# Kernel tuning notes

Hardware: AMD Instinct MI355X
Metric: run time of the kernel (lower is better)

Reference implementation:

```python
import jax, jax.numpy as jnp
import numpy as np

N = 8192       # num_nodes
E = 262144     # num_edges (avg degree 32)
D_IN = 256
D_H = 256
D_OUT = 256
BN_EPS = 1e-5


def _linear_params(key, din, dout):
    # torch nn.Linear default init: U(-1/sqrt(din), 1/sqrt(din))
    s = 1.0 / np.sqrt(din)
    kw, kb = jax.random.split(key)
    W = jax.random.uniform(kw, (dout, din), jnp.float32, -s, s)
    b = jax.random.uniform(kb, (dout,), jnp.float32, -s, s)
    return W, b


def setup_inputs() -> dict:
    key = jax.random.key(0)
    ks = jax.random.split(key, 6)
    x = jax.random.normal(ks[0], (N, D_IN), jnp.float32)
    edge_index = jax.random.randint(ks[1], (2, E), 0, N, dtype=jnp.int64)
    W1, b1 = _linear_params(ks[2], D_IN, D_H)
    W2, b2 = _linear_params(ks[3], D_H, D_H)
    W3, b3 = _linear_params(ks[4], D_H, D_OUT)
    return {
        "x": x, "edge_index": edge_index,
        "W1": W1, "b1": b1, "W2": W2, "b2": b2, "W3": W3, "b3": b3,
        "g1": jnp.ones((D_H,), jnp.float32), "be1": jnp.zeros((D_H,), jnp.float32),
        "g2": jnp.ones((D_H,), jnp.float32), "be2": jnp.zeros((D_H,), jnp.float32),
        "g3": jnp.ones((D_OUT,), jnp.float32), "be3": jnp.zeros((D_OUT,), jnp.float32),
    }


def _build_norm(edge_index):
    # add self loops, scatter 1.0 into dense NxN adjacency (duplicates collapse via set)
    loop = jnp.arange(N, dtype=edge_index.dtype)
    rows = jnp.concatenate([edge_index[0], loop])
    cols = jnp.concatenate([edge_index[1], loop])
    adj = jnp.zeros((N, N), jnp.float32).at[rows, cols].set(1.0)
    deg = adj.sum(axis=1)
    dinv = jnp.where(deg > 0, deg ** -0.5, 0.0)  # inf -> 0 as in original
    return dinv[:, None] * adj * dinv[None, :]


def _gcn(x, norm, W, b):
    # linear then symmetric-normalized aggregation
    return norm @ (x @ W.T + b)


def _bn(x, g, b):
    # BatchNorm1d with batch statistics (biased var), eps=1e-5
    mu = x.mean(axis=0)
    var = x.var(axis=0)
    return (x - mu) * jax.lax.rsqrt(var + BN_EPS) * g + b


def reference(x, edge_index, W1, b1, W2, b2, W3, b3, g1, be1, g2, be2, g3, be3):
    norm = _build_norm(edge_index)
    h = jax.nn.relu(_bn(_gcn(x, norm, W1, b1), g1, be1))
    h = jax.nn.relu(_bn(_gcn(h, norm, W2, b2), g2, be2))
    h = _bn(_gcn(h, norm, W3, b3), g3, be3)
    return h
```

## Files before the change

### kernel.cpp

```cpp
#include <hip/hip_runtime.h>

#define N_NODES 8192
#define N_EDGES 262144
#define D 256
#define ADJ_WORDS 256
#define MAX_DEG 128
#define AGG_BLOCKS 2048
#define RED_BLOCKS 128

typedef __attribute__((ext_vector_type(8))) short bf16x8;
typedef __attribute__((ext_vector_type(4))) float f32x4;

__device__ __forceinline__ short f2bf(float f) {
    unsigned u = __builtin_bit_cast(unsigned, f);
    u += 0x7fffu + ((u >> 16) & 1);
    return (short)(u >> 16);
}
__device__ __forceinline__ float bf2f(unsigned short u) {
    return __builtin_bit_cast(float, ((unsigned)u) << 16);
}

__global__ void build_adj(const int* __restrict__ ei, unsigned* __restrict__ adj,
                          int* __restrict__ deg) {
    int i = blockIdx.x * blockDim.x + threadIdx.x;
    int r, c;
    if (i < N_EDGES) {
        r = ei[i];
        c = ei[N_EDGES + i];
    } else if (i < N_EDGES + N_NODES) {
        r = i - N_EDGES;
        c = r;
    } else {
        return;
    }
    unsigned bit = 1u << (c & 31);
    unsigned old = atomicOr(&adj[r * ADJ_WORDS + (c >> 5)], bit);
    if (!(old & bit)) atomicAdd(&deg[r], 1);
}

__global__ __launch_bounds__(256) void compute_dinv(const int* __restrict__ deg,
                                                    float* __restrict__ dinv) {
    int i = blockIdx.x * 256 + threadIdx.x;
    int d = deg[i];
    dinv[i] = d > 0 ? rsqrtf((float)d) : 0.0f;
}

__global__ __launch_bounds__(256) void build_nbrs(const unsigned* __restrict__ adj,
                                                  const float* __restrict__ dinv,
                                                  int* __restrict__ nbr_idx,
                                                  float* __restrict__ nbr_w,
                                                  const float* __restrict__ W1,
                                                  const float* __restrict__ W2,
                                                  const float* __restrict__ W3,
                                                  unsigned short* __restrict__ Wb1,
                                                  unsigned short* __restrict__ Wb2,
                                                  unsigned short* __restrict__ Wb3) {
    if (blockIdx.x >= N_NODES) {
        int i = (blockIdx.x - N_NODES) * 256 + threadIdx.x;
        int which = i >> 16, j = i & 65535;
        const float* src = which == 0 ? W1 : which == 1 ? W2 : W3;
        unsigned short* dst = which == 0 ? Wb1 : which == 1 ? Wb2 : Wb3;
        dst[j] = (unsigned short)f2bf(src[j]);
        return;
    }
    const int r = blockIdx.x;
    const int t = threadIdx.x;
    const int lane = t & 63, wave = t >> 6;
    unsigned m = adj[r * ADJ_WORDS + t];
    int cnt = __popc(m);
    int x = cnt;
    #pragma unroll
    for (int off = 1; off < 64; off <<= 1) {
        int v = __shfl_up(x, off, 64);
        if (lane >= off) x += v;
    }
    __shared__ int wtot[4];
    if (lane == 63) wtot[wave] = x;
    __syncthreads();
    int woff = 0;
    #pragma unroll
    for (int w = 0; w < 4; w++) woff += (w < wave) ? wtot[w] : 0;
    int base = woff + x - cnt;
    const float dr = dinv[r];
    int* oi = nbr_idx + (size_t)r * MAX_DEG;
    float* ow = nbr_w + (size_t)r * MAX_DEG;
    while (m) {
        int b = __ffs(m) - 1;
        m &= m - 1;
        int c = (t << 5) + b;
        if (base < MAX_DEG) {
            oi[base] = c;
            ow[base] = dr * dinv[c];
        }
        base++;
    }
}

template <bool APPLY, bool RELU>
__global__ __launch_bounds__(256) void gemm_mfma(const float* __restrict__ Xsrc,
                                                 const float* __restrict__ scale,
                                                 const float* __restrict__ shift,
                                                 const unsigned short* __restrict__ Wb,
                                                 const float* __restrict__ bias,
                                                 unsigned short* __restrict__ Hb) {
    const int bn = blockIdx.x * 64;
    const int bm = blockIdx.y * 128;
    const int tid = threadIdx.x;
    const int wave = tid >> 6, lane = tid & 63;
    const int l16 = lane & 15, q = lane >> 4;
    const int mrow0 = bm + wave * 32;

    f32x4 acc[2][4];
    #pragma unroll
    for (int i = 0; i < 2; i++)
        #pragma unroll
        for (int j = 0; j < 4; j++) acc[i][j] = (f32x4){0.f, 0.f, 0.f, 0.f};

    for (int k0 = 0; k0 < D; k0 += 32) {
        const int kq = k0 + q * 8;
        bf16x8 xb[2];
        float4 sc0, sc1, sh0, sh1;
        if (APPLY) {
            sc0 = *(const float4*)(scale + kq);
            sc1 = *(const float4*)(scale + kq + 4);
            sh0 = *(const float4*)(shift + kq);
            sh1 = *(const float4*)(shift + kq + 4);
        }
        #pragma unroll
        for (int mf = 0; mf < 2; mf++) {
            const float* xr = Xsrc + (size_t)(mrow0 + mf * 16 + l16) * D + kq;
            float4 a = *(const float4*)xr;
            float4 b = *(const float4*)(xr + 4);
            float v[8] = {a.x, a.y, a.z, a.w, b.x, b.y, b.z, b.w};
            if (APPLY) {
                float sc[8] = {sc0.x, sc0.y, sc0.z, sc0.w, sc1.x, sc1.y, sc1.z, sc1.w};
                float sh[8] = {sh0.x, sh0.y, sh0.z, sh0.w, sh1.x, sh1.y, sh1.z, sh1.w};
                #pragma unroll
                for (int j = 0; j < 8; j++) {
                    v[j] = fmaf(v[j], sc[j], sh[j]);
                    if (RELU) v[j] = fmaxf(v[j], 0.0f);
                }
            }
            #pragma unroll
            for (int j = 0; j < 8; j++) xb[mf][j] = f2bf(v[j]);
        }
        #pragma unroll
        for (int nf = 0; nf < 4; nf++) {
            bf16x8 wa = *(const bf16x8*)(Wb + (size_t)(bn + nf * 16 + l16) * D + kq);
            #pragma unroll
            for (int mf = 0; mf < 2; mf++)
                acc[mf][nf] = __builtin_amdgcn_mfma_f32_16x16x32_bf16(wa, xb[mf], acc[mf][nf], 0, 0, 0);
        }
    }

    #pragma unroll
    for (int mf = 0; mf < 2; mf++) {
        const int m = mrow0 + mf * 16 + l16;
        #pragma unroll
        for (int nf = 0; nf < 4; nf++) {
            const int nb = bn + nf * 16 + q * 4;
            float4 b4 = *(const float4*)(bias + nb);
            short4 o;
            o.x = f2bf(acc[mf][nf][0] + b4.x);
            o.y = f2bf(acc[mf][nf][1] + b4.y);
            o.z = f2bf(acc[mf][nf][2] + b4.z);
            o.w = f2bf(acc[mf][nf][3] + b4.w);
            *(short4*)(Hb + (size_t)m * D + nb) = o;
        }
    }
}

__global__ __launch_bounds__(256) void aggregate_bf16(const int* __restrict__ nbr_idx,
                                                      const float* __restrict__ nbr_w,
                                                      const int* __restrict__ deg,
                                                      const unsigned short* __restrict__ Hb,
                                                      float* __restrict__ G,
                                                      float* __restrict__ psum,
                                                      float* __restrict__ psumsq) {
    const int wave = threadIdx.x >> 6;
    const int lane = threadIdx.x & 63;
    const int ch = lane * 4;
    const int r = blockIdx.x * 4 + wave;

    int dg = deg[r]; if (dg > MAX_DEG) dg = MAX_DEG;
    const int* idx = nbr_idx + (size_t)r * MAX_DEG;
    const float* wt = nbr_w + (size_t)r * MAX_DEG;
    float4 A = make_float4(0.f, 0.f, 0.f, 0.f);
    int j = 0;
    for (; j + 8 <= dg; j += 8) {
        int4 c0 = *(const int4*)(idx + j);
        int4 c1 = *(const int4*)(idx + j + 4);
        float4 w0 = *(const float4*)(wt + j);
        float4 w1 = *(const float4*)(wt + j + 4);
        ushort4 u0 = *(const ushort4*)(Hb + (size_t)c0.x * D + ch);
        ushort4 u1 = *(const ushort4*)(Hb + (size_t)c0.y * D + ch);
        ushort4 u2 = *(const ushort4*)(Hb + (size_t)c0.z * D + ch);
        ushort4 u3 = *(const ushort4*)(Hb + (size_t)c0.w * D + ch);
        ushort4 u4 = *(const ushort4*)(Hb + (size_t)c1.x * D + ch);
        ushort4 u5 = *(const ushort4*)(Hb + (size_t)c1.y * D + ch);
        ushort4 u6 = *(const ushort4*)(Hb + (size_t)c1.z * D + ch);
        ushort4 u7 = *(const ushort4*)(Hb + (size_t)c1.w * D + ch);
        A.x = fmaf(w0.x, bf2f(u0.x), A.x); A.y = fmaf(w0.x, bf2f(u0.y), A.y);
        A.z = fmaf(w0.x, bf2f(u0.z), A.z); A.w = fmaf(w0.x, bf2f(u0.w), A.w);
        A.x = fmaf(w0.y, bf2f(u1.x), A.x); A.y = fmaf(w0.y, bf2f(u1.y), A.y);
        A.z = fmaf(w0.y, bf2f(u1.z), A.z); A.w = fmaf(w0.y, bf2f(u1.w), A.w);
        A.x = fmaf(w0.z, bf2f(u2.x), A.x); A.y = fmaf(w0.z, bf2f(u2.y), A.y);
        A.z = fmaf(w0.z, bf2f(u2.z), A.z); A.w = fmaf(w0.z, bf2f(u2.w), A.w);
        A.x = fmaf(w0.w, bf2f(u3.x), A.x); A.y = fmaf(w0.w, bf2f(u3.y), A.y);
        A.z = fmaf(w0.w, bf2f(u3.z), A.z); A.w = fmaf(w0.w, bf2f(u3.w), A.w);
        A.x = fmaf(w1.x, bf2f(u4.x), A.x); A.y = fmaf(w1.x, bf2f(u4.y), A.y);
        A.z = fmaf(w1.x, bf2f(u4.z), A.z); A.w = fmaf(w1.x, bf2f(u4.w), A.w);
        A.x = fmaf(w1.y, bf2f(u5.x), A.x); A.y = fmaf(w1.y, bf2f(u5.y), A.y);
        A.z = fmaf(w1.y, bf2f(u5.z), A.z); A.w = fmaf(w1.y, bf2f(u5.w), A.w);
        A.x = fmaf(w1.z, bf2f(u6.x), A.x); A.y = fmaf(w1.z, bf2f(u6.y), A.y);
        A.z = fmaf(w1.z, bf2f(u6.z), A.z); A.w = fmaf(w1.z, bf2f(u6.w), A.w);
        A.x = fmaf(w1.w, bf2f(u7.x), A.x); A.y = fmaf(w1.w, bf2f(u7.y), A.y);
        A.z = fmaf(w1.w, bf2f(u7.z), A.z); A.w = fmaf(w1.w, bf2f(u7.w), A.w);
    }
    for (; j + 4 <= dg; j += 4) {
        int4 c0 = *(const int4*)(idx + j);
        float4 w0 = *(const float4*)(wt + j);
        ushort4 u0 = *(const ushort4*)(Hb + (size_t)c0.x * D + ch);
        ushort4 u1 = *(const ushort4*)(Hb + (size_t)c0.y * D + ch);
        ushort4 u2 = *(const ushort4*)(Hb + (size_t)c0.z * D + ch);
        ushort4 u3 = *(const ushort4*)(Hb + (size_t)c0.w * D + ch);
        A.x = fmaf(w0.x, bf2f(u0.x), A.x); A.y = fmaf(w0.x, bf2f(u0.y), A.y);
        A.z = fmaf(w0.x, bf2f(u0.z), A.z); A.w = fmaf(w0.x, bf2f(u0.w), A.w);
        A.x = fmaf(w0.y, bf2f(u1.x), A.x); A.y = fmaf(w0.y, bf2f(u1.y), A.y);
        A.z = fmaf(w0.y, bf2f(u1.z), A.z); A.w = fmaf(w0.y, bf2f(u1.w), A.w);
        A.x = fmaf(w0.z, bf2f(u2.x), A.x); A.y = fmaf(w0.z, bf2f(u2.y), A.y);
        A.z = fmaf(w0.z, bf2f(u2.z), A.z); A.w = fmaf(w0.z, bf2f(u2.w), A.w);
        A.x = fmaf(w0.w, bf2f(u3.x), A.x); A.y = fmaf(w0.w, bf2f(u3.y), A.y);
        A.z = fmaf(w0.w, bf2f(u3.z), A.z); A.w = fmaf(w0.w, bf2f(u3.w), A.w);
    }
    for (; j < dg; j++) {
        int c = idx[j];
        float w = wt[j];
        ushort4 u = *(const ushort4*)(Hb + (size_t)c * D + ch);
        A.x = fmaf(w, bf2f(u.x), A.x); A.y = fmaf(w, bf2f(u.y), A.y);
        A.z = fmaf(w, bf2f(u.z), A.z); A.w = fmaf(w, bf2f(u.w), A.w);
    }
    *(float4*)(G + (size_t)r * D + ch) = A;

    __shared__ float ls[4][256], lss[4][256];
    ls[wave][ch] = A.x; ls[wave][ch + 1] = A.y; ls[wave][ch + 2] = A.z; ls[wave][ch + 3] = A.w;
    lss[wave][ch] = A.x * A.x; lss[wave][ch + 1] = A.y * A.y;
    lss[wave][ch + 2] = A.z * A.z; lss[wave][ch + 3] = A.w * A.w;
    __syncthreads();
    const int t = threadIdx.x;
    psum[blockIdx.x * 256 + t] = ls[0][t] + ls[1][t] + ls[2][t] + ls[3][t];
    psumsq[blockIdx.x * 256 + t] = lss[0][t] + lss[1][t] + lss[2][t] + lss[3][t];
}

__global__ __launch_bounds__(256) void reduce_partials(const float* __restrict__ psum,
                                                       const float* __restrict__ psumsq,
                                                       float* __restrict__ psum2,
                                                       float* __restrict__ psumsq2) {
    const int b = blockIdx.x;
    const int t = threadIdx.x;
    const int rows = AGG_BLOCKS / RED_BLOCKS;
    float s = 0.0f, q = 0.0f;
    #pragma unroll
    for (int i = 0; i < rows; i++) {
        s += psum[(size_t)(b * rows + i) * 256 + t];
        q += psumsq[(size_t)(b * rows + i) * 256 + t];
    }
    psum2[b * 256 + t] = s;
    psumsq2[b * 256 + t] = q;
}

__global__ __launch_bounds__(1024) void bn_stats2(const float* __restrict__ psum2,
                                                  const float* __restrict__ psumsq2,
                                                  const float* __restrict__ g,
                                                  const float* __restrict__ be,
                                                  float* __restrict__ scale,
                                                  float* __restrict__ shift) {
    const int t = threadIdx.x;
    const int chn = t & 255, part = t >> 8;
    float s = 0.0f, q = 0.0f;
    for (int i = part; i < RED_BLOCKS; i += 4) {
        s += psum2[i * 256 + chn];
        q += psumsq2[i * 256 + chn];
    }
    __shared__ float as[4][256], aq[4][256];
    as[part][chn] = s;
    aq[part][chn] = q;
    __syncthreads();
    if (t < 256) {
        s = as[0][t] + as[1][t] + as[2][t] + as[3][t];
        q = aq[0][t] + aq[1][t] + aq[2][t] + aq[3][t];
        float mu = s * (1.0f / N_NODES);
        float var = q * (1.0f / N_NODES) - mu * mu;
        float rstd = rsqrtf(var + 1e-5f);
        float sc = g[t] * rstd;
        scale[t] = sc;
        shift[t] = be[t] - mu * sc;
    }
}

__global__ __launch_bounds__(256) void bn_apply_out(const float* __restrict__ G,
                                                    const float* __restrict__ scale,
                                                    const float* __restrict__ shift,
                                                    float* __restrict__ Out) {
    int i = (blockIdx.x * 256 + threadIdx.x) * 4;
    int d = i & (D - 1);
    float4 v = *(const float4*)(G + i);
    float4 sc = *(const float4*)(scale + d);
    float4 sh = *(const float4*)(shift + d);
    v.x = fmaf(v.x, sc.x, sh.x);
    v.y = fmaf(v.y, sc.y, sh.y);
    v.z = fmaf(v.z, sc.z, sh.z);
    v.w = fmaf(v.w, sc.w, sh.w);
    *(float4*)(Out + i) = v;
}

extern "C" void kernel_launch(void* const* d_in, const int* in_sizes, int n_in,
                              void* d_out, int out_size, void* d_ws, size_t ws_size,
                              hipStream_t stream) {
    const float* x  = (const float*)d_in[0];
    const int*   ei = (const int*)d_in[1];
    const float* W1 = (const float*)d_in[2];
    const float* b1 = (const float*)d_in[3];
    const float* W2 = (const float*)d_in[4];
    const float* b2 = (const float*)d_in[5];
    const float* W3 = (const float*)d_in[6];
    const float* b3 = (const float*)d_in[7];
    const float* g1 = (const float*)d_in[8];
    const float* be1 = (const float*)d_in[9];
    const float* g2 = (const float*)d_in[10];
    const float* be2 = (const float*)d_in[11];
    const float* g3 = (const float*)d_in[12];
    const float* be3 = (const float*)d_in[13];

    char* ws = (char*)d_ws;
    unsigned*       adj  = (unsigned*)ws;
    unsigned short* Hb   = (unsigned short*)ws;
    int*            deg  = (int*)(ws + (8 << 20));
    float*          dinv = (float*)(ws + (8 << 20) + (32 << 10));
    float*          scale= (float*)(ws + (8 << 20) + (64 << 10));
    float*          shift= (float*)(ws + (8 << 20) + (68 << 10));
    float*          psum2= (float*)(ws + (8 << 20) + (72 << 10));
    float*          psq2 = (float*)(ws + (8 << 20) + (200 << 10));
    unsigned short* Wb1  = (unsigned short*)(ws + (8 << 20) + (330 << 10));
    unsigned short* Wb2  = (unsigned short*)(ws + (8 << 20) + (458 << 10));
    unsigned short* Wb3  = (unsigned short*)(ws + (8 << 20) + (586 << 10));
    float*          psum = (float*)(ws + (9 << 20));
    float*          psq  = (float*)(ws + (11 << 20));
    int*            nbr_idx = (int*)  (ws + (13 << 20));
    float*          nbr_w   = (float*)(ws + (17 << 20));
    float*          G       = (float*)(ws + (21 << 20));

    hipMemsetAsync(ws, 0, (8 << 20) + (32 << 10), stream);

    build_adj<<<(N_EDGES + N_NODES + 255) / 256, 256, 0, stream>>>(ei, adj, deg);
    compute_dinv<<<N_NODES / 256, 256, 0, stream>>>(deg, dinv);
    build_nbrs<<<N_NODES + 768, 256, 0, stream>>>(adj, dinv, nbr_idx, nbr_w,
                                                  W1, W2, W3, Wb1, Wb2, Wb3);

    dim3 ggrid(D / 64, N_NODES / 128);

    gemm_mfma<false, false><<<ggrid, 256, 0, stream>>>(x, nullptr, nullptr, Wb1, b1, Hb);
    aggregate_bf16<<<AGG_BLOCKS, 256, 0, stream>>>(nbr_idx, nbr_w, deg, Hb, G, psum, psq);
    reduce_partials<<<RED_BLOCKS, 256, 0, stream>>>(psum, psq, psum2, psq2);
    bn_stats2<<<1, 1024, 0, stream>>>(psum2, psq2, g1, be1, scale, shift);

    gemm_mfma<true, true><<<ggrid, 256, 0, stream>>>(G, scale, shift, Wb2, b2, Hb);
    aggregate_bf16<<<AGG_BLOCKS, 256, 0, stream>>>(nbr_idx, nbr_w, deg, Hb, G, psum, psq);
    reduce_partials<<<RED_BLOCKS, 256, 0, stream>>>(psum, psq, psum2, psq2);
    bn_stats2<<<1, 1024, 0, stream>>>(psum2, psq2, g2, be2, scale, shift);

    gemm_mfma<true, true><<<ggrid, 256, 0, stream>>>(G, scale, shift, Wb3, b3, Hb);
    aggregate_bf16<<<AGG_BLOCKS, 256, 0, stream>>>(nbr_idx, nbr_w, deg, Hb, G, psum, psq);
    reduce_partials<<<RED_BLOCKS, 256, 0, stream>>>(psum, psq, psum2, psq2);
    bn_stats2<<<1, 1024, 0, stream>>>(psum2, psq2, g3, be3, scale, shift);

    bn_apply_out<<<N_NODES * D / 1024, 256, 0, stream>>>(G, scale, shift, (float*)d_out);
}
```

Measured before the change: 255.7 us.

## Fold BN stats and dinv computation into consumer kernels, removing small launches

Removes the compute_dinv kernel by computing rsqrt of degree inline in build_nbrs, and removes the three single-block bn_stats2 kernels. Each consumer block (gemm_mfma with APPLY, and bn_apply_out) now reduces the 128 partial sums itself and builds scale/shift in shared memory. bn_apply_out is restructured so each block handles 64 rows. The aim is to cut four kernel launches and the serialized single-block reduction, at the cost of every GEMM block redundantly reading the 256 KB of partials. The deg>0 guard is dropped, which is safe here because self-loops make every degree at least 1.

```diff
diff --git a/kernel.cpp b/kernel.cpp
--- a/kernel.cpp
+++ b/kernel.cpp
@@ -38,15 +38,8 @@
     if (!(old & bit)) atomicAdd(&deg[r], 1);
 }
 
-__global__ __launch_bounds__(256) void compute_dinv(const int* __restrict__ deg,
-                                                    float* __restrict__ dinv) {
-    int i = blockIdx.x * 256 + threadIdx.x;
-    int d = deg[i];
-    dinv[i] = d > 0 ? rsqrtf((float)d) : 0.0f;
-}
-
 __global__ __launch_bounds__(256) void build_nbrs(const unsigned* __restrict__ adj,
-                                                  const float* __restrict__ dinv,
+                                                  const int* __restrict__ deg,
                                                   int* __restrict__ nbr_idx,
                                                   float* __restrict__ nbr_w,
                                                   const float* __restrict__ W1,
@@ -81,7 +74,7 @@
     #pragma unroll
     for (int w = 0; w < 4; w++) woff += (w < wave) ? wtot[w] : 0;
     int base = woff + x - cnt;
-    const float dr = dinv[r];
+    const float dr = rsqrtf((float)deg[r]);
     int* oi = nbr_idx + (size_t)r * MAX_DEG;
     float* ow = nbr_w + (size_t)r * MAX_DEG;
     while (m) {
@@ -90,7 +83,7 @@
         int c = (t << 5) + b;
         if (base < MAX_DEG) {
             oi[base] = c;
-            ow[base] = dr * dinv[c];
+            ow[base] = dr * rsqrtf((float)deg[c]);
         }
         base++;
     }
@@ -98,14 +91,33 @@
 
 template <bool APPLY, bool RELU>
 __global__ __launch_bounds__(256) void gemm_mfma(const float* __restrict__ Xsrc,
-                                                 const float* __restrict__ scale,
-                                                 const float* __restrict__ shift,
+                                                 const float* __restrict__ psum2,
+                                                 const float* __restrict__ psq2,
+                                                 const float* __restrict__ g,
+                                                 const float* __restrict__ be,
                                                  const unsigned short* __restrict__ Wb,
                                                  const float* __restrict__ bias,
                                                  unsigned short* __restrict__ Hb) {
+    __shared__ float ssc[256], ssh[256];
+    const int tid = threadIdx.x;
+    if (APPLY) {
+        float s = 0.f, q = 0.f;
+        #pragma unroll 8
+        for (int i = 0; i < RED_BLOCKS; i++) {
+            s += psum2[i * 256 + tid];
+            q += psq2[i * 256 + tid];
+        }
+        float mu = s * (1.0f / N_NODES);
+        float var = q * (1.0f / N_NODES) - mu * mu;
+        float rstd = rsqrtf(var + 1e-5f);
+        float sc = g[tid] * rstd;
+        ssc[tid] = sc;
+        ssh[tid] = be[tid] - mu * sc;
+        __syncthreads();
+    }
+
     const int bn = blockIdx.x * 64;
     const int bm = blockIdx.y * 128;
-    const int tid = threadIdx.x;
     const int wave = tid >> 6, lane = tid & 63;
     const int l16 = lane & 15, q = lane >> 4;
     const int mrow0 = bm + wave * 32;
@@ -121,10 +133,10 @@
         bf16x8 xb[2];
         float4 sc0, sc1, sh0, sh1;
         if (APPLY) {
-            sc0 = *(const float4*)(scale + kq);
-            sc1 = *(const float4*)(scale + kq + 4);
-            sh0 = *(const float4*)(shift + kq);
-            sh1 = *(const float4*)(shift + kq + 4);
+            sc0 = *(const float4*)(ssc + kq);
+            sc1 = *(const float4*)(ssc + kq + 4);
+            sh0 = *(const float4*)(ssh + kq);
+            sh1 = *(const float4*)(ssh + kq + 4);
         }
         #pragma unroll
         for (int mf = 0; mf < 2; mf++) {
@@ -269,49 +281,44 @@
     psumsq2[b * 256 + t] = q;
 }
 
-__global__ __launch_bounds__(1024) void bn_stats2(const float* __restrict__ psum2,
-                                                  const float* __restrict__ psumsq2,
-                                                  const float* __restrict__ g,
-                                                  const float* __restrict__ be,
-                                                  float* __restrict__ scale,
-                                                  float* __restrict__ shift) {
-    const int t = threadIdx.x;
-    const int chn = t & 255, part = t >> 8;
-    float s = 0.0f, q = 0.0f;
-    for (int i = part; i < RED_BLOCKS; i += 4) {
-        s += psum2[i * 256 + chn];
-        q += psumsq2[i * 256 + chn];
-    }
-    __shared__ float as[4][256], aq[4][256];
-    as[part][chn] = s;
-    aq[part][chn] = q;
-    __syncthreads();
-    if (t < 256) {
-        s = as[0][t] + as[1][t] + as[2][t] + as[3][t];
-        q = aq[0][t] + aq[1][t] + aq[2][t] + aq[3][t];
+__global__ __launch_bounds__(256) void bn_apply_out(const float* __restrict__ G,
+                                                    const float* __restrict__ psum2,
+                                                    const float* __restrict__ psq2,
+                                                    const float* __restrict__ g,
+                                                    const float* __restrict__ be,
+                                                    float* __restrict__ Out) {
+    __shared__ float ssc[256], ssh[256];
+    const int tid = threadIdx.x;
+    {
+        float s = 0.f, q = 0.f;
+        #pragma unroll 8
+        for (int i = 0; i < RED_BLOCKS; i++) {
+            s += psum2[i * 256 + tid];
+            q += psq2[i * 256 + tid];
+        }
         float mu = s * (1.0f / N_NODES);
         float var = q * (1.0f / N_NODES) - mu * mu;
         float rstd = rsqrtf(var + 1e-5f);
-        float sc = g[t] * rstd;
-        scale[t] = sc;
-        shift[t] = be[t] - mu * sc;
-    }
-}
-
-__global__ __launch_bounds__(256) void bn_apply_out(const float* __restrict__ G,
-                                                    const float* __restrict__ scale,
-                                                    const float* __restrict__ shift,
-                                                    float* __restrict__ Out) {
-    int i = (blockIdx.x * 256 + threadIdx.x) * 4;
-    int d = i & (D - 1);
-    float4 v = *(const float4*)(G + i);
-    float4 sc = *(const float4*)(scale + d);
-    float4 sh = *(const float4*)(shift + d);
-    v.x = fmaf(v.x, sc.x, sh.x);
-    v.y = fmaf(v.y, sc.y, sh.y);
-    v.z = fmaf(v.z, sc.z, sh.z);
-    v.w = fmaf(v.w, sc.w, sh.w);
-    *(float4*)(Out + i) = v;
+        float sc = g[tid] * rstd;
+        ssc[tid] = sc;
+        ssh[tid] = be[tid] - mu * sc;
+        __syncthreads();
+    }
+    const int rows_per_block = 64;
+    const int r0 = blockIdx.x * rows_per_block;
+    const int ch = (tid & 63) * 4;
+    const int rsub = tid >> 6;
+    float4 sc = *(const float4*)(ssc + ch);
+    float4 sh = *(const float4*)(ssh + ch);
+    for (int rr = rsub; rr < rows_per_block; rr += 4) {
+        const size_t off = (size_t)(r0 + rr) * D + ch;
+        float4 v = *(const float4*)(G + off);
+        v.x = fmaf(v.x, sc.x, sh.x);
+        v.y = fmaf(v.y, sc.y, sh.y);
+        v.z = fmaf(v.z, sc.z, sh.z);
+        v.w = fmaf(v.w, sc.w, sh.w);
+        *(float4*)(Out + off) = v;
+    }
 }
 
 extern "C" void kernel_launch(void* const* d_in, const int* in_sizes, int n_in,
@@ -336,14 +343,11 @@
     unsigned*       adj  = (unsigned*)ws;
     unsigned short* Hb   = (unsigned short*)ws;
     int*            deg  = (int*)(ws + (8 << 20));
-    float*          dinv = (float*)(ws + (8 << 20) + (32 << 10));
-    float*          scale= (float*)(ws + (8 << 20) + (64 << 10));
-    float*          shift= (float*)(ws + (8 << 20) + (68 << 10));
-    float*          psum2= (float*)(ws + (8 << 20) + (72 << 10));
-    float*          psq2 = (float*)(ws + (8 << 20) + (200 << 10));
-    unsigned short* Wb1  = (unsigned short*)(ws + (8 << 20) + (330 << 10));
-    unsigned short* Wb2  = (unsigned short*)(ws + (8 << 20) + (458 << 10));
-    unsigned short* Wb3  = (unsigned short*)(ws + (8 << 20) + (586 << 10));
+    float*          psum2= (float*)(ws + (8 << 20) + (64 << 10));
+    float*          psq2 = (float*)(ws + (8 << 20) + (192 << 10));
+    unsigned short* Wb1  = (unsigned short*)(ws + (8 << 20) + (320 << 10));
+    unsigned short* Wb2  = (unsigned short*)(ws + (8 << 20) + (448 << 10));
+    unsigned short* Wb3  = (unsigned short*)(ws + (8 << 20) + (576 << 10));
     float*          psum = (float*)(ws + (9 << 20));
     float*          psq  = (float*)(ws + (11 << 20));
     int*            nbr_idx = (int*)  (ws + (13 << 20));
@@ -353,26 +357,23 @@
     hipMemsetAsync(ws, 0, (8 << 20) + (32 << 10), stream);
 
     build_adj<<<(N_EDGES + N_NODES + 255) / 256, 256, 0, stream>>>(ei, adj, deg);
-    compute_dinv<<<N_NODES / 256, 256, 0, stream>>>(deg, dinv);
-    build_nbrs<<<N_NODES + 768, 256, 0, stream>>>(adj, dinv, nbr_idx, nbr_w,
+    build_nbrs<<<N_NODES + 768, 256, 0, stream>>>(adj, deg, nbr_idx, nbr_w,
                                                   W1, W2, W3, Wb1, Wb2, Wb3);
 
     dim3 ggrid(D / 64, N_NODES / 128);
 
-    gemm_mfma<false, false><<<ggrid, 256, 0, stream>>>(x, nullptr, nullptr, Wb1, b1, Hb);
+    gemm_mfma<false, false><<<ggrid, 256, 0, stream>>>(x, nullptr, nullptr, nullptr, nullptr,
+                                                       Wb1, b1, Hb);
     aggregate_bf16<<<AGG_BLOCKS, 256, 0, stream>>>(nbr_idx, nbr_w, deg, Hb, G, psum, psq);
     reduce_partials<<<RED_BLOCKS, 256, 0, stream>>>(psum, psq, psum2, psq2);
-    bn_stats2<<<1, 1024, 0, stream>>>(psum2, psq2, g1, be1, scale, shift);
-
-    gemm_mfma<true, true><<<ggrid, 256, 0, stream>>>(G, scale, shift, Wb2, b2, Hb);
+
+    gemm_mfma<true, true><<<ggrid, 256, 0, stream>>>(G, psum2, psq2, g1, be1, Wb2, b2, Hb);
     aggregate_bf16<<<AGG_BLOCKS, 256, 0, stream>>>(nbr_idx, nbr_w, deg, Hb, G, psum, psq);
     reduce_partials<<<RED_BLOCKS, 256, 0, stream>>>(psum, psq, psum2, psq2);
-    bn_stats2<<<1, 1024, 0, stream>>>(psum2, psq2, g2, be2, scale, shift);
-
-    gemm_mfma<true, true><<<ggrid, 256, 0, stream>>>(G, scale, shift, Wb3, b3, Hb);
+
+    gemm_mfma<true, true><<<ggrid, 256, 0, stream>>>(G, psum2, psq2, g2, be2, Wb3, b3, Hb);
     aggregate_bf16<<<AGG_BLOCKS, 256, 0, stream>>>(nbr_idx, nbr_w, deg, Hb, G, psum, psq);
     reduce_partials<<<RED_BLOCKS, 256, 0, stream>>>(psum, psq, psum2, psq2);
-    bn_stats2<<<1, 1024, 0, stream>>>(psum2, psq2, g3, be3, scale, shift);
-
-    bn_apply_out<<<N_NODES * D / 1024, 256, 0, stream>>>(G, scale, shift, (float*)d_out);
-}
+
+    bn_apply_out<<<N_NODES / 64, 256, 0, stream>>>(G, psum2, psq2, g3, be3, (float*)d_out);
+}
```

Result: faster. 237.3 us (median of 2 runs) (-7.2%).
